# Kernel optimization log

Measured on AMD Instinct MI355X. Metric: run time of the kernel, lower is better.

Reference implementation:

```python
import jax, jax.numpy as jnp
import numpy as np

N_DYADIC = 0   # dyadic refinement order (init kwarg n)
SOLVER = 0     # first-order explicit finite-difference scheme (init kwarg solver)


def _solve_goursat(inc):
    """Solve Goursat PDE K_{p+1,q+1} = K_{p+1,q} + K_{p,q+1} - K_{p,q} + inc[p,q]*K_{p,q}
    with boundary K[0,:] = K[:,0] = 1. inc: [B, P, Q] -> returns K[P,Q] per pair: [B]."""
    B, P, Q = inc.shape
    dt = inc.dtype
    ones_b = jnp.ones((B,), dt)

    def row_step(prev_row, inc_row):
        # prev_row: [B, Q+1] = K[p, :]; inc_row: [B, Q]
        def col_step(k_left, t):
            k_diag, k_up, a = t  # K[p,q], K[p,q+1], inc[p,q], each [B]
            k_new = k_up + (k_left - k_diag) + a * k_diag
            return k_new, k_new
        xs = (prev_row[:, :-1].T, prev_row[:, 1:].T, inc_row.T)  # [Q, B] each
        _, tail = jax.lax.scan(col_step, ones_b, xs)              # tail: [Q, B]
        new_row = jnp.concatenate([ones_b[:, None], tail.T], axis=1)
        return new_row, None

    final_row, _ = jax.lax.scan(row_step, jnp.ones((B, Q + 1), dt), jnp.swapaxes(inc, 0, 1))
    return final_row[:, -1]


def _sig_kernel_gram(X, Y, n=N_DYADIC):
    """Signature-kernel Gram matrix. X: [A, M, D], Y: [B, N, D] -> [A, B]."""
    dX = X[:, 1:, :] - X[:, :-1, :]          # [A, M-1, D]
    dY = Y[:, 1:, :] - Y[:, :-1, :]          # [B, N-1, D]
    Minc = jnp.einsum('apd,bqd->abpq', dX, dY)  # pairwise increment inner products
    f = 2 ** n
    if f > 1:  # dyadic grid refinement: split each cell into f*f subcells
        Minc = jnp.repeat(jnp.repeat(Minc, f, axis=2), f, axis=3) / (f * f)
    A, B, P, Q = Minc.shape
    K = _solve_goursat(Minc.reshape(A * B, P, Q))
    return K.reshape(A, B)


def setup_inputs() -> dict:
    key = jax.random.key(0)
    kx, ky = jax.random.split(key)
    SCALE = 0.05  # small Brownian-like increments keep the exponential kernel tame
    X = jnp.cumsum(SCALE * jax.random.normal(kx, (64, 128, 64), dtype=jnp.float32), axis=1)
    Y = jnp.cumsum(SCALE * jax.random.normal(ky, (64, 128, 64), dtype=jnp.float32), axis=1)
    return {"X": X, "Y": Y}


def reference(X, Y):
    K_XX = _sig_kernel_gram(X, X)
    K_YY = _sig_kernel_gram(Y, Y)
    K_XY = _sig_kernel_gram(X, Y)
    dist = jnp.mean(K_XX) + jnp.mean(K_YY) - 2.0 * jnp.mean(K_XY)
    return jnp.mean((X[:, 0, :] - Y[:, 0, :]) ** 2) + dist
```

## Files before the change

kernel.cpp:

```cpp
#include <hip/hip_runtime.h>
#include <math.h>

#define DD 64
#define MM 128
#define RSW 132
#define BUFW 2112

typedef float  f32x4v __attribute__((ext_vector_type(4)));
typedef __bf16 bf16x8 __attribute__((ext_vector_type(8)));

#define FOR8(F) F(0) F(1) F(2) F(3) F(4) F(5) F(6) F(7)

union FragU { unsigned int u[4]; bf16x8 v; };

__device__ __forceinline__ unsigned cvtpk(float lo, float hi) {
    unsigned r;
    asm("v_cvt_pk_bf16_f32 %0, %1, %2" : "=v"(r) : "v"(lo), "v"(hi));
    return r;
}

__device__ __forceinline__ bf16x8 dfrag_hi(const float* __restrict__ r0,
                                           const float* __restrict__ r1) {
    float4 a0 = *(const float4*)r0, a1 = *(const float4*)(r0 + 4);
    float4 b0 = *(const float4*)r1, b1 = *(const float4*)(r1 + 4);
    FragU f;
    f.u[0] = cvtpk(b0.x - a0.x, b0.y - a0.y);
    f.u[1] = cvtpk(b0.z - a0.z, b0.w - a0.w);
    f.u[2] = cvtpk(b1.x - a1.x, b1.y - a1.y);
    f.u[3] = cvtpk(b1.z - a1.z, b1.w - a1.w);
    return f.v;
}

template<int CTRL, int RM, bool BC>
__device__ __forceinline__ float dpp_add(float x) {
    int t = __builtin_amdgcn_update_dpp(0, __float_as_int(x), CTRL, RM, 0xf, BC);
    return x + __int_as_float(t);
}
__device__ __forceinline__ float wave_incl_scan(float x) {
    x = dpp_add<0x111, 0xf, true >(x);
    x = dpp_add<0x112, 0xf, true >(x);
    x = dpp_add<0x114, 0xf, true >(x);
    x = dpp_add<0x118, 0xf, true >(x);
    x = dpp_add<0x142, 0xa, false>(x);
    x = dpp_add<0x143, 0xc, false>(x);
    return x;
}

__global__ __launch_bounds__(128, 4) void sig_goursat_kernel(
        const float* __restrict__ X, const float* __restrict__ Y,
        float* __restrict__ Kout)
{
    const int bid = blockIdx.x;
    int g, a, b;
    if (bid < 4160) {
        g = bid < 2080 ? 0 : 1;
        const int t = bid - g * 2080;
        float sq = sqrtf(4160.25f - 2.0f * (float)t);
        a = (int)(64.5f - sq);
        if (a < 0) a = 0; if (a > 63) a = 63;
        while (a > 0  && (a * (129 - a)) / 2 > t) --a;
        while (a < 63 && ((a + 1) * (128 - a)) / 2 <= t) ++a;
        b = a + (t - (a * (129 - a)) / 2);
    } else {
        const int t = bid - 4160;
        g = 2; a = t >> 6; b = t & 63;
    }

    const int tid  = threadIdx.x;
    const int wid  = tid >> 6;
    const int lane = tid & 63;

    __shared__ float buf[2][BUFW];

    if (wid == 0) {
        const float* __restrict__ U = (g == 1 ? Y : X) + (size_t)a * (MM * DD);
        const float* __restrict__ V = (g == 0 ? X : Y) + (size_t)b * (MM * DD);
        const int l15  = lane & 15;
        const int k8   = (lane >> 4) * 8;
        const int rowg = (lane >> 4) * 4;
        const int wbase = rowg * RSW + l15;

#define TBDECL(ct) bf16x8 tb0_##ct, tb1_##ct;
        FOR8(TBDECL)
#define TBUILD(ct) { int brow_ = ct * 16 + l15; if (brow_ > 126) brow_ = 126; \
        const float* vp_ = V + (size_t)brow_ * DD + k8; \
        tb0_##ct = dfrag_hi(vp_,      vp_ + DD); \
        tb1_##ct = dfrag_hi(vp_ + 32, vp_ + DD + 32); }
        FOR8(TBUILD)

#define CTSTEP(ct) { f32x4v c = {0.f, 0.f, 0.f, 0.f}; \
        c = __builtin_amdgcn_mfma_f32_16x16x32_bf16(ak0, tb0_##ct, c, 0, 0, 0); \
        c = __builtin_amdgcn_mfma_f32_16x16x32_bf16(ak1, tb1_##ct, c, 0, 0, 0); \
        const int w_ = wbase + ct * 16; \
        bp[w_]         = c[0]; \
        bp[w_ + RSW]   = c[1]; \
        bp[w_ + 2*RSW] = c[2]; \
        bp[w_ + 3*RSW] = c[3]; }

        for (int band = 0; band < 8; ++band) {
            int arow = band * 16 + l15; if (arow > 126) arow = 126;
            const float* ap = U + (size_t)arow * DD + k8;
            bf16x8 ak0 = dfrag_hi(ap,      ap + DD);
            bf16x8 ak1 = dfrag_hi(ap + 32, ap + DD + 32);
            float* bp = buf[band & 1];
            FOR8(CTSTEP)
            __syncthreads();
        }
    } else {
        float KL0 = 1.0f, KL1 = 1.0f;

#define SCANROW1(e) { \
        const float m0 = e.x * KL0; \
        const float m1 = e.y * KL1; \
        const float t_ = m0 + m1; \
        const float S_ = wave_incl_scan(t_); \
        const float ex = S_ - t_; \
        KL1 += ex + m0; \
        KL0 += ex; }

        for (int band = 0; band < 7; ++band) {
            __syncthreads();
            const float2* pl = (const float2*)&buf[band & 1][2 * lane];
            float2 e = pl[0];
            float2 f = pl[66];
            #pragma unroll
            for (int r = 0; r < 14; ++r) {
                float2 n = pl[(r + 2) * 66];
                SCANROW1(e)
                e = f; f = n;
            }
            SCANROW1(e)
            SCANROW1(f)
        }
        {
            __syncthreads();
            const float2* pl = (const float2*)&buf[1][2 * lane];
            float2 e = pl[0];
            float2 f = pl[66];
            #pragma unroll
            for (int r = 0; r < 13; ++r) {
                float2 n = pl[(r + 2) * 66];
                SCANROW1(e)
                e = f; f = n;
            }
            SCANROW1(e)
            SCANROW1(f)
        }

        if (lane == 63) Kout[(size_t)g * 4096 + a * 64 + b] = KL1;
    }
}

__global__ void sig_reduce_kernel(const float* __restrict__ X,
                                  const float* __restrict__ Y,
                                  const float* __restrict__ Kws,
                                  float* __restrict__ out)
{
    const int t = threadIdx.x;
    double accK = 0.0, acc2 = 0.0;
    for (int i = t; i < 4096; i += 256) {
        const int a = i >> 6, b = i & 63;
        if (a <= b) {
            const double w = (a == b) ? 1.0 : 2.0;
            accK += w * (double)Kws[i];
            accK += w * (double)Kws[4096 + i];
        }
        accK -= 2.0 * (double)Kws[8192 + i];
        const float df = X[(size_t)a * (MM * DD) + b] - Y[(size_t)a * (MM * DD) + b];
        acc2 += (double)df * (double)df;
    }
    __shared__ double red[256];
    red[t] = accK / 4096.0 + acc2 / 4096.0;
    __syncthreads();
    for (int s = 128; s > 0; s >>= 1) {
        if (t < s) red[t] += red[t + s];
        __syncthreads();
    }
    if (t == 0) out[0] = (float)red[0];
}

extern "C" void kernel_launch(void* const* d_in, const int* in_sizes, int n_in,
                              void* d_out, int out_size, void* d_ws, size_t ws_size,
                              hipStream_t stream) {
    const float* X = (const float*)d_in[0];
    const float* Y = (const float*)d_in[1];
    float* Kws = (float*)d_ws;
    float* out = (float*)d_out;

    sig_goursat_kernel<<<dim3(8256), dim3(128), 0, stream>>>(X, Y, Kws);
    sig_reduce_kernel<<<dim3(1), dim3(256), 0, stream>>>(X, Y, Kws, out);
}
```

Baseline: 141.3 us.

## Fuse MFMA producer and scan consumer into one wave per pair

Each path pair is now handled by a single wavefront that computes the increment band with MFMA and then scans it. Four pairs are packed per 256-thread block, replacing the old producer/consumer wave split that used block-wide __syncthreads. The band tile is stored in LDS as packed bf16 pairs, with a DPP quad swap used to interleave columns, which halves LDS traffic and footprint. The trade-off is that MFMA and scan work are serialized within each wave instead of overlapping across two waves, and the increments stored for the scan are now rounded to bf16.

```diff
diff --git a/kernel.cpp b/kernel.cpp
--- a/kernel.cpp
+++ b/kernel.cpp
@@ -3,8 +3,8 @@
 
 #define DD 64
 #define MM 128
-#define RSW 132
-#define BUFW 2112
+#define PSTR 66
+#define PWORDS (16 * PSTR)
 
 typedef float  f32x4v __attribute__((ext_vector_type(4)));
 typedef __bf16 bf16x8 __attribute__((ext_vector_type(8)));
@@ -17,6 +17,11 @@
     unsigned r;
     asm("v_cvt_pk_bf16_f32 %0, %1, %2" : "=v"(r) : "v"(lo), "v"(hi));
     return r;
+}
+
+__device__ __forceinline__ float qswap(float x) {
+    int t = __builtin_amdgcn_update_dpp(0, __float_as_int(x), 0xB1, 0xF, 0xF, true);
+    return __int_as_float(t);
 }
 
 __device__ __forceinline__ bf16x8 dfrag_hi(const float* __restrict__ r0,
@@ -46,109 +51,107 @@
     return x;
 }
 
-__global__ __launch_bounds__(128, 4) void sig_goursat_kernel(
+__global__ __launch_bounds__(256, 4) void sig_goursat_kernel(
         const float* __restrict__ X, const float* __restrict__ Y,
         float* __restrict__ Kout)
 {
-    const int bid = blockIdx.x;
-    int g, a, b;
-    if (bid < 4160) {
-        g = bid < 2080 ? 0 : 1;
-        const int t = bid - g * 2080;
-        float sq = sqrtf(4160.25f - 2.0f * (float)t);
-        a = (int)(64.5f - sq);
-        if (a < 0) a = 0; if (a > 63) a = 63;
-        while (a > 0  && (a * (129 - a)) / 2 > t) --a;
-        while (a < 63 && ((a + 1) * (128 - a)) / 2 <= t) ++a;
-        b = a + (t - (a * (129 - a)) / 2);
-    } else {
-        const int t = bid - 4160;
-        g = 2; a = t >> 6; b = t & 63;
-    }
-
     const int tid  = threadIdx.x;
     const int wid  = tid >> 6;
     const int lane = tid & 63;
+    const int t    = blockIdx.x * 4 + wid;
 
-    __shared__ float buf[2][BUFW];
+    int g, a, b;
+    if (t < 4160) {
+        g = t < 2080 ? 0 : 1;
+        const int u = t - g * 2080;
+        float sq = sqrtf(4160.25f - 2.0f * (float)u);
+        a = (int)(64.5f - sq);
+        if (a < 0) a = 0; if (a > 63) a = 63;
+        while (a > 0  && (a * (129 - a)) / 2 > u) --a;
+        while (a < 63 && ((a + 1) * (128 - a)) / 2 <= u) ++a;
+        b = a + (u - (a * (129 - a)) / 2);
+    } else {
+        const int u = t - 4160;
+        g = 2; a = u >> 6; b = u & 63;
+    }
 
-    if (wid == 0) {
-        const float* __restrict__ U = (g == 1 ? Y : X) + (size_t)a * (MM * DD);
-        const float* __restrict__ V = (g == 0 ? X : Y) + (size_t)b * (MM * DD);
-        const int l15  = lane & 15;
-        const int k8   = (lane >> 4) * 8;
-        const int rowg = (lane >> 4) * 4;
-        const int wbase = rowg * RSW + l15;
+    const float* __restrict__ U = (g == 1 ? Y : X) + (size_t)a * (MM * DD);
+    const float* __restrict__ V = (g == 0 ? X : Y) + (size_t)b * (MM * DD);
+
+    const int l15  = lane & 15;
+    const int k8   = (lane >> 4) * 8;
+    const int rowg = (lane >> 4) * 4;
+    const int par  = l15 & 1;
+
+    __shared__ unsigned incL[4][PWORDS];
+    unsigned* __restrict__ plane = incL[wid];
 
 #define TBDECL(ct) bf16x8 tb0_##ct, tb1_##ct;
-        FOR8(TBDECL)
+    FOR8(TBDECL)
 #define TBUILD(ct) { int brow_ = ct * 16 + l15; if (brow_ > 126) brow_ = 126; \
         const float* vp_ = V + (size_t)brow_ * DD + k8; \
         tb0_##ct = dfrag_hi(vp_,      vp_ + DD); \
         tb1_##ct = dfrag_hi(vp_ + 32, vp_ + DD + 32); }
-        FOR8(TBUILD)
+    FOR8(TBUILD)
 
-#define CTSTEP(ct) { f32x4v c = {0.f, 0.f, 0.f, 0.f}; \
+    float KL0 = 1.0f, KL1 = 1.0f;
+
+    const int wA = (rowg + 2 * par) * PSTR + (l15 >> 1);
+    const int wB = wA + PSTR;
+
+#define CTSTEP(ct) { \
+        f32x4v c = {0.f, 0.f, 0.f, 0.f}; \
         c = __builtin_amdgcn_mfma_f32_16x16x32_bf16(ak0, tb0_##ct, c, 0, 0, 0); \
         c = __builtin_amdgcn_mfma_f32_16x16x32_bf16(ak1, tb1_##ct, c, 0, 0, 0); \
-        const int w_ = wbase + ct * 16; \
-        bp[w_]         = c[0]; \
-        bp[w_ + RSW]   = c[1]; \
-        bp[w_ + 2*RSW] = c[2]; \
-        bp[w_ + 3*RSW] = c[3]; }
+        const float n0 = qswap(c[0]); const float n1 = qswap(c[1]); \
+        const float n2 = qswap(c[2]); const float n3 = qswap(c[3]); \
+        const float loA = par ? n2 : c[0]; const float hiA = par ? c[2] : n0; \
+        const float loB = par ? n3 : c[1]; const float hiB = par ? c[3] : n1; \
+        plane[wA + ct * 8] = cvtpk(loA, hiA); \
+        plane[wB + ct * 8] = cvtpk(loB, hiB); }
 
-        for (int band = 0; band < 8; ++band) {
-            int arow = band * 16 + l15; if (arow > 126) arow = 126;
-            const float* ap = U + (size_t)arow * DD + k8;
-            bf16x8 ak0 = dfrag_hi(ap,      ap + DD);
-            bf16x8 ak1 = dfrag_hi(ap + 32, ap + DD + 32);
-            float* bp = buf[band & 1];
-            FOR8(CTSTEP)
-            __syncthreads();
-        }
-    } else {
-        float KL0 = 1.0f, KL1 = 1.0f;
-
-#define SCANROW1(e) { \
-        const float m0 = e.x * KL0; \
-        const float m1 = e.y * KL1; \
+#define SCANROW(w) { \
+        const float iE = __uint_as_float((w) << 16); \
+        const float iO = __uint_as_float((w) & 0xffff0000u); \
+        const float m0 = iE * KL0; \
+        const float m1 = iO * KL1; \
         const float t_ = m0 + m1; \
         const float S_ = wave_incl_scan(t_); \
         const float ex = S_ - t_; \
         KL1 += ex + m0; \
         KL0 += ex; }
 
-        for (int band = 0; band < 7; ++band) {
-            __syncthreads();
-            const float2* pl = (const float2*)&buf[band & 1][2 * lane];
-            float2 e = pl[0];
-            float2 f = pl[66];
-            #pragma unroll
-            for (int r = 0; r < 14; ++r) {
-                float2 n = pl[(r + 2) * 66];
-                SCANROW1(e)
-                e = f; f = n;
-            }
-            SCANROW1(e)
-            SCANROW1(f)
+    const unsigned* __restrict__ prow = plane + lane;
+
+    for (int band = 0; band < 8; ++band) {
+        int arow = band * 16 + l15; if (arow > 126) arow = 126;
+        const float* ap = U + (size_t)arow * DD + k8;
+        bf16x8 ak0 = dfrag_hi(ap,      ap + DD);
+        bf16x8 ak1 = dfrag_hi(ap + 32, ap + DD + 32);
+
+        FOR8(CTSTEP)
+
+        unsigned e = prow[0];
+        unsigned f = prow[PSTR];
+        #pragma unroll
+        for (int r = 0; r < 13; ++r) {
+            unsigned n = prow[(r + 2) * PSTR];
+            SCANROW(e)
+            e = f; f = n;
         }
-        {
-            __syncthreads();
-            const float2* pl = (const float2*)&buf[1][2 * lane];
-            float2 e = pl[0];
-            float2 f = pl[66];
-            #pragma unroll
-            for (int r = 0; r < 13; ++r) {
-                float2 n = pl[(r + 2) * 66];
-                SCANROW1(e)
-                e = f; f = n;
-            }
-            SCANROW1(e)
-            SCANROW1(f)
+        if (band < 7) {
+            unsigned n = prow[15 * PSTR];
+            SCANROW(e)
+            e = f; f = n;
+            SCANROW(e)
+            SCANROW(f)
+        } else {
+            SCANROW(e)
+            SCANROW(f)
         }
+    }
 
-        if (lane == 63) Kout[(size_t)g * 4096 + a * 64 + b] = KL1;
-    }
+    if (lane == 63) Kout[(size_t)g * 4096 + a * 64 + b] = KL1;
 }
 
 __global__ void sig_reduce_kernel(const float* __restrict__ X,
@@ -187,6 +190,6 @@
     float* Kws = (float*)d_ws;
     float* out = (float*)d_out;
 
-    sig_goursat_kernel<<<dim3(8256), dim3(128), 0, stream>>>(X, Y, Kws);
+    sig_goursat_kernel<<<dim3(2064), dim3(256), 0, stream>>>(X, Y, Kws);
     sig_reduce_kernel<<<dim3(1), dim3(256), 0, stream>>>(X, Y, Kws, out);
 }
```

New measurement: 155.1 us. 9.8% more time.
